# Kernel optimization log

Hardware: AMD Instinct MI355X
Metric: run time of the kernel (lower is better)

The kernel has to match this reference:

```python
import jax, jax.numpy as jnp
import numpy as np

EPS = 1e-5


def conv2d(x, w, b, pad):
    # x: [B,C,H,W], w: [O,I,kh,kw]
    out = jax.lax.conv_general_dilated(
        x, w, window_strides=(1, 1), padding=[(pad, pad), (pad, pad)],
        dimension_numbers=('NCHW', 'OIHW', 'NCHW'))
    return out + b[None, :, None, None]


def bilinear_gather(xf, py, px, H, W):
    # xf: [B,C,H*W]; py,px: [B,H,W] float sampling positions
    # zero padding outside the image (torchvision deform_conv2d semantics)
    y0 = jnp.floor(py)
    x0 = jnp.floor(px)
    wy = py - y0
    wx = px - x0
    y0i = y0.astype(jnp.int32)
    x0i = x0.astype(jnp.int32)
    B, C = xf.shape[0], xf.shape[1]
    acc = jnp.zeros((B, C, H, W), xf.dtype)
    for dy, wyv in ((0, 1.0 - wy), (1, wy)):
        for dx, wxv in ((0, 1.0 - wx), (1, wx)):
            yi = y0i + dy
            xi = x0i + dx
            valid = ((yi >= 0) & (yi < H) & (xi >= 0) & (xi < W)).astype(xf.dtype)
            idx = jnp.clip(yi, 0, H - 1) * W + jnp.clip(xi, 0, W - 1)  # [B,H,W]
            g = jnp.take_along_axis(xf, idx.reshape(B, 1, H * W), axis=2)
            g = g.reshape(B, C, H, W)
            acc = acc + g * (wyv * wxv * valid)[:, None]
    return acc


def deform_conv2d(x, offset, w, b, k):
    # x: [B,C,H,W]; offset: [B,2*k*k,H,W] ((dy,dx) pairs per kernel tap)
    B, C, H, W = x.shape
    pad = k // 2
    gy = jnp.arange(H, dtype=x.dtype)[None, :, None]
    gx = jnp.arange(W, dtype=x.dtype)[None, None, :]
    xf = x.reshape(B, C, H * W)
    out = jnp.zeros((B, w.shape[0], H, W), x.dtype)
    for i in range(k):
        for j in range(k):
            kk = i * k + j
            py = gy + (i - pad) + offset[:, 2 * kk]
            px = gx + (j - pad) + offset[:, 2 * kk + 1]
            samp = bilinear_gather(xf, py, px, H, W)  # [B,C,H,W]
            out = out + jnp.einsum('bchw,oc->bohw', samp, w[:, :, i, j])
    return out + b[None, :, None, None]


def setup_inputs() -> dict:
    key = jax.random.key(0)
    ks = jax.random.split(key, 16)
    B, C, H, W = 4, 64, 192, 192
    k = 3
    hid = max(1, C // 16)
    d = {}
    d['x'] = jax.random.normal(ks[0], (B, C, H, W), jnp.float32)
    # offset-prediction conv (3x3, pad 1) -> 2*k*k channels
    d['off_w'] = jax.random.normal(ks[1], (2 * k * k, C, 3, 3), jnp.float32) * 0.02
    d['off_b'] = jax.random.normal(ks[2], (2 * k * k,), jnp.float32) * 0.02
    # deformable conv weights (C->C, kxk)
    d['dw'] = jax.random.normal(ks[3], (C, C, k, k), jnp.float32) * 0.05
    d['db'] = jax.random.normal(ks[4], (C,), jnp.float32) * 0.05
    # BatchNorm (eval: running stats)
    d['bn_gamma'] = jnp.ones((C,), jnp.float32) + 0.1 * jax.random.normal(ks[5], (C,), jnp.float32)
    d['bn_beta'] = 0.1 * jax.random.normal(ks[6], (C,), jnp.float32)
    d['bn_mean'] = 0.1 * jax.random.normal(ks[7], (C,), jnp.float32)
    d['bn_var'] = jnp.ones((C,), jnp.float32)
    # channel attention: 1x1 squeeze / excite
    d['ca_w1'] = jax.random.normal(ks[8], (hid, C, 1, 1), jnp.float32) * 0.1
    d['ca_b1'] = jnp.zeros((hid,), jnp.float32)
    d['ca_w2'] = jax.random.normal(ks[9], (C, hid, 1, 1), jnp.float32) * 0.1
    d['ca_b2'] = jnp.zeros((C,), jnp.float32)
    # spatial attention: 7x7 conv -> 1 channel
    d['sa_w'] = jax.random.normal(ks[10], (1, C, 7, 7), jnp.float32) * 0.02
    d['sa_b'] = jnp.zeros((1,), jnp.float32)
    return d


def reference(x, off_w, off_b, dw, db, bn_gamma, bn_beta, bn_mean, bn_var,
              ca_w1, ca_b1, ca_w2, ca_b2, sa_w, sa_b):
    k = 3
    # extract: DeformableConv2d + BatchNorm2d
    offset = conv2d(x, off_w, off_b, pad=1)
    h = deform_conv2d(x, offset, dw, db, k)
    inv = jax.lax.rsqrt(bn_var + EPS)
    h = (h - bn_mean[None, :, None, None]) * (bn_gamma * inv)[None, :, None, None] \
        + bn_beta[None, :, None, None]
    # channel attention
    pooled = jnp.mean(h, axis=(2, 3), keepdims=True)  # [B,C,1,1]
    cw = conv2d(pooled, ca_w1, ca_b1, pad=0)
    cw = jax.nn.relu(cw)
    cw = conv2d(cw, ca_w2, ca_b2, pad=0)
    cw = jax.nn.sigmoid(cw)
    h = h * cw
    # spatial attention (7x7 conv, pad 3)
    sw = jax.nn.sigmoid(conv2d(h, sa_w, sa_b, pad=3))  # [B,1,H,W]
    h = h * sw
    return h
```

## Files before the change

### kernel.cpp

```cpp
#include <hip/hip_runtime.h>
#include <hip/hip_bf16.h>

#define H_  192
#define W_  192
#define HW  36864
#define B_  4

typedef __attribute__((ext_vector_type(8))) short short8;
typedef __attribute__((ext_vector_type(4))) float f32x4;
typedef __attribute__((ext_vector_type(4))) unsigned int u32x4;
typedef unsigned short ushort_t;
typedef unsigned int uint_t;

__device__ __forceinline__ ushort_t f2bf(float v) {
    uint_t u = __builtin_bit_cast(uint_t, v);
    u += 0x7FFFu + ((u >> 16) & 1u);
    return (ushort_t)(u >> 16);
}
__device__ __forceinline__ float bflo(uint_t u) {
    uint_t w = u << 16; return __builtin_bit_cast(float, w);
}
__device__ __forceinline__ float bfhi(uint_t u) {
    uint_t w = u & 0xFFFF0000u; return __builtin_bit_cast(float, w);
}
__device__ __forceinline__ short8 zero8() {
    u32x4 z = {0u, 0u, 0u, 0u};
    return __builtin_bit_cast(short8, z);
}

__device__ __forceinline__ void glds16(const ushort_t* src, void* lds_base) {
    __builtin_amdgcn_global_load_lds(
        (const __attribute__((address_space(1))) void*)src,
        (__attribute__((address_space(3))) void*)lds_base, 16, 0, 0);
}

__global__ void prep_kernel(const float* __restrict__ dw, const float* __restrict__ db,
                            const float* __restrict__ g, const float* __restrict__ be,
                            const float* __restrict__ mu, const float* __restrict__ var,
                            const float* __restrict__ ow,
                            ushort_t* __restrict__ w_bf, ushort_t* __restrict__ w_off,
                            float* __restrict__ scale, float* __restrict__ shift) {
    int idx = blockIdx.x * 256 + threadIdx.x;
    if (idx < 36864) {
        int tap = idx >> 12, o = (idx >> 6) & 63, c = idx & 63;
        w_bf[idx] = f2bf(dw[(o * 64 + c) * 9 + tap]);
    }
    int idx2 = idx - 36864;
    if (idx2 >= 0 && idx2 < 18432) {
        int tap = idx2 >> 11, o = (idx2 >> 6) & 31, c = idx2 & 63;
        w_off[idx2] = (o < 18) ? f2bf(ow[(o * 64 + c) * 9 + tap]) : (ushort_t)0;
    }
    if (idx < 64) {
        float s = g[idx] * rsqrtf(var[idx] + 1e-5f);
        scale[idx] = s;
        shift[idx] = (db[idx] - mu[idx]) * s + be[idx];
    }
}

__global__ __launch_bounds__(256) void transpose_kernel(const float* __restrict__ x,
                                                        ushort_t* __restrict__ x_t) {
    __shared__ uint_t tlds[256 * 33];
    int tid = threadIdx.x;
    int b = blockIdx.x / 144;
    int p0 = (blockIdx.x % 144) * 256;
    ushort_t* ts = (ushort_t*)tlds;
    for (int c = 0; c < 64; ++c) {
        float v = x[((size_t)(b * 64 + c)) * HW + p0 + tid];
        ts[tid * 66 + c] = f2bf(v);
    }
    __syncthreads();
#pragma unroll
    for (int j = 0; j < 8; ++j) {
        int chunk = j * 256 + tid;
        int pl = chunk >> 3, s = chunk & 7;
        int bd = pl * 33 + s * 4;
        u32x4 v = {tlds[bd], tlds[bd + 1], tlds[bd + 2], tlds[bd + 3]};
        ((u32x4*)x_t)[(size_t)(b * HW + p0) * 8 + chunk] = v;
    }
}

__device__ __forceinline__ u32x4 prd(const ushort_t* patch, int q, int slot) {
    return *(const u32x4*)((const char*)patch + q * 128 + ((slot ^ (q & 7)) << 4));
}

__device__ __forceinline__ bool corner_setup2(float ody, float odx,
                                              int ybase, int xbase, int ytop, int xleft,
                                              int* q, int* g, float* w) {
    float py = (float)ybase + ody;
    float px = (float)xbase + odx;
    float fy = floorf(py), fx = floorf(px);
    int y0 = (int)fy, x0 = (int)fx;
    float wy = py - fy, wx = px - fx;
    int y0c = min(max(y0, 0), H_ - 1), y1c = min(max(y0 + 1, 0), H_ - 1);
    int x0c = min(max(x0, 0), W_ - 1), x1c = min(max(x0 + 1, 0), W_ - 1);
    float vy0 = (y0 >= 0 && y0 < H_) ? 1.f : 0.f;
    float vy1 = (y0 + 1 >= 0 && y0 + 1 < H_) ? 1.f : 0.f;
    float vx0 = (x0 >= 0 && x0 < W_) ? 1.f : 0.f;
    float vx1 = (x0 + 1 >= 0 && x0 + 1 < W_) ? 1.f : 0.f;
    w[0] = (1.f - wy) * (1.f - wx) * vy0 * vx0;
    w[1] = (1.f - wy) * wx * vy0 * vx1;
    w[2] = wy * (1.f - wx) * vy1 * vx0;
    w[3] = wy * wx * vy1 * vx1;
    g[0] = (y0c * W_ + x0c) * 64; g[1] = (y0c * W_ + x1c) * 64;
    g[2] = (y1c * W_ + x0c) * 64; g[3] = (y1c * W_ + x1c) * 64;
    int iy0 = y0c - ytop, iy1 = y1c - ytop;
    int ix0 = x0c - xleft, ix1 = x1c - xleft;
    q[0] = iy0 * 40 + ix0; q[1] = iy0 * 40 + ix1;
    q[2] = iy1 * 40 + ix0; q[3] = iy1 * 40 + ix1;
    return ((unsigned)iy0 <= 11u) & ((unsigned)iy1 <= 11u) &
           ((unsigned)ix0 <= 39u) & ((unsigned)ix1 <= 39u);
}

__device__ __forceinline__ short8 interp_compute(const u32x4* buf, const float* w) {
    short8 r;
#pragma unroll
    for (int q = 0; q < 4; ++q) {
        float lo = w[0] * bflo(buf[0][q]) + w[1] * bflo(buf[1][q]) +
                   w[2] * bflo(buf[2][q]) + w[3] * bflo(buf[3][q]);
        float hi = w[0] * bfhi(buf[0][q]) + w[1] * bfhi(buf[1][q]) +
                   w[2] * bfhi(buf[2][q]) + w[3] * bfhi(buf[3][q]);
        __hip_bfloat162 h2 = __float22bfloat162_rn(make_float2(lo, hi));
        uint_t p;
        __builtin_memcpy(&p, &h2, 4);
        ((uint_t*)&r)[q] = p;
    }
    return r;
}

__global__ __launch_bounds__(384, 3) void deform_fused_kernel(
    const ushort_t* __restrict__ x_t, const ushort_t* __restrict__ w_off,
    const float* __restrict__ ob, const ushort_t* __restrict__ w_bf,
    const float* __restrict__ scale_g, const float* __restrict__ shift_g,
    float* __restrict__ out) {
    __shared__ __align__(16) ushort_t patch[480 * 64];

    int tid = threadIdx.x;
    int lane = tid & 63, w = tid >> 6;
    int tile = (blockIdx.x & 7) * 96 + (blockIdx.x >> 3);
    int b = tile / 192;
    int rem = tile % 192;
    int y0 = (rem / 6) * 6;
    int x0 = (rem % 6) * 32;
    int ytop = y0 - 3, xleft = x0 - 4;

    int ln = lane & 15, kg = lane >> 4;
    int yw = y0 + w;
    int xA = x0 + ln, xB = xA + 16;
    const ushort_t* xt_b = x_t + (size_t)b * (HW * 64);

    {
        char* pbase = (char*)patch;
#pragma unroll
        for (int t = 0; t < 10; ++t) {
            int g = t * 384 + tid;
            int q = g >> 3, sp = g & 7;
            int i = q / 40, j = q - i * 40;
            int pr = min(max(ytop + i, 0), H_ - 1);
            int pc = min(max(xleft + j, 0), W_ - 1);
            int s = sp ^ (q & 7);
            glds16(xt_b + (pr * W_ + pc) * 64 + s * 8, pbase + (t * 6 + w) * 1024);
        }
    }
    asm volatile("s_waitcnt vmcnt(0)" ::: "memory");
    __syncthreads();

    f32x4 ao[2][2];
#pragma unroll
    for (int i = 0; i < 2; ++i)
#pragma unroll
        for (int j = 0; j < 2; ++j) ao[i][j] = (f32x4){0.f, 0.f, 0.f, 0.f};

    for (int tap = 0; tap < 9; ++tap) {
        int ti = tap / 3 - 1, tj = tap % 3 - 1;
        bool vA = ((unsigned)(yw + ti) < (unsigned)H_) && ((unsigned)(xA + tj) < (unsigned)W_);
        bool vB = ((unsigned)(yw + ti) < (unsigned)H_) && ((unsigned)(xB + tj) < (unsigned)W_);
        int qA = (w + ti + 3) * 40 + (ln + 4 + tj);
        int qB = qA + 16;
        const ushort_t* wt = w_off + tap * 2048;
#pragma unroll
        for (int ks = 0; ks < 2; ++ks) {
            int ch = ks * 32 + kg * 8;
            int slot = kg + ks * 4;
            short8 a0 = *(const short8*)(wt + ln * 64 + ch);
            short8 a1 = *(const short8*)(wt + (16 + ln) * 64 + ch);
            short8 bA = vA ? __builtin_bit_cast(short8, prd(patch, qA, slot)) : zero8();
            short8 bB = vB ? __builtin_bit_cast(short8, prd(patch, qB, slot)) : zero8();
            ao[0][0] = __builtin_amdgcn_mfma_f32_16x16x32_bf16(a0, bA, ao[0][0], 0, 0, 0);
            ao[0][1] = __builtin_amdgcn_mfma_f32_16x16x32_bf16(a0, bB, ao[0][1], 0, 0, 0);
            ao[1][0] = __builtin_amdgcn_mfma_f32_16x16x32_bf16(a1, bA, ao[1][0], 0, 0, 0);
            ao[1][1] = __builtin_amdgcn_mfma_f32_16x16x32_bf16(a1, bB, ao[1][1], 0, 0, 0);
        }
    }

    float offA[18], offB[18];
#pragma unroll
    for (int m = 0; m < 18; ++m) {
        int src = (((m >> 2) & 3) << 4) | ln;
        float bias = ob[m];
        offA[m] = __shfl(ao[m >> 4][0][m & 3], src, 64) + bias;
        offB[m] = __shfl(ao[m >> 4][1][m & 3], src, 64) + bias;
    }

    f32x4 acc[4][2];
#pragma unroll
    for (int mt = 0; mt < 4; ++mt)
#pragma unroll
        for (int nt = 0; nt < 2; ++nt) acc[mt][nt] = (f32x4){0.f, 0.f, 0.f, 0.f};

#pragma unroll
    for (int tap = 0; tap < 9; ++tap) {
        int ti = tap / 3 - 1, tj = tap % 3 - 1;
        int qA[4], qB[4], gA[4], gB[4];
        float wA[4], wB[4];
        bool inA = corner_setup2(offA[2 * tap], offA[2 * tap + 1],
                                 yw + ti, xA + tj, ytop, xleft, qA, gA, wA);
        bool inB = corner_setup2(offB[2 * tap], offB[2 * tap + 1],
                                 yw + ti, xB + tj, ytop, xleft, qB, gB, wB);
        const ushort_t* wt = w_bf + tap * 4096;
#pragma unroll
        for (int ks = 0; ks < 2; ++ks) {
            int ch = ks * 32 + kg * 8;
            int slot = kg + ks * 4;
            u32x4 cA[4], cB[4];
            if (__builtin_expect(inA, 1)) {
#pragma unroll
                for (int c = 0; c < 4; ++c) cA[c] = prd(patch, qA[c], slot);
            } else {
#pragma unroll
                for (int c = 0; c < 4; ++c) cA[c] = *(const u32x4*)(xt_b + gA[c] + ch);
            }
            if (__builtin_expect(inB, 1)) {
#pragma unroll
                for (int c = 0; c < 4; ++c) cB[c] = prd(patch, qB[c], slot);
            } else {
#pragma unroll
                for (int c = 0; c < 4; ++c) cB[c] = *(const u32x4*)(xt_b + gB[c] + ch);
            }
            short8 fA = interp_compute(cA, wA);
            short8 fB = interp_compute(cB, wB);
            short8 a0 = *(const short8*)(wt + (0 + ln) * 64 + ch);
            short8 a1 = *(const short8*)(wt + (16 + ln) * 64 + ch);
            short8 a2 = *(const short8*)(wt + (32 + ln) * 64 + ch);
            short8 a3 = *(const short8*)(wt + (48 + ln) * 64 + ch);
            acc[0][0] = __builtin_amdgcn_mfma_f32_16x16x32_bf16(a0, fA, acc[0][0], 0, 0, 0);
            acc[0][1] = __builtin_amdgcn_mfma_f32_16x16x32_bf16(a0, fB, acc[0][1], 0, 0, 0);
            acc[1][0] = __builtin_amdgcn_mfma_f32_16x16x32_bf16(a1, fA, acc[1][0], 0, 0, 0);
            acc[1][1] = __builtin_amdgcn_mfma_f32_16x16x32_bf16(a1, fB, acc[1][1], 0, 0, 0);
            acc[2][0] = __builtin_amdgcn_mfma_f32_16x16x32_bf16(a2, fA, acc[2][0], 0, 0, 0);
            acc[2][1] = __builtin_amdgcn_mfma_f32_16x16x32_bf16(a2, fB, acc[2][1], 0, 0, 0);
            acc[3][0] = __builtin_amdgcn_mfma_f32_16x16x32_bf16(a3, fA, acc[3][0], 0, 0, 0);
            acc[3][1] = __builtin_amdgcn_mfma_f32_16x16x32_bf16(a3, fB, acc[3][1], 0, 0, 0);
        }
    }

#pragma unroll
    for (int mt = 0; mt < 4; ++mt) {
#pragma unroll
        for (int r = 0; r < 4; ++r) {
            int m = mt * 16 + kg * 4 + r;
            float sc = scale_g[m], sh = shift_g[m];
            size_t orow = (size_t)(b * 64 + m) * HW + yw * 192 + x0 + ln;
            out[orow] = acc[mt][0][r] * sc + sh;
            out[orow + 16] = acc[mt][1][r] * sc + sh;
        }
    }
}

__global__ __launch_bounds__(256) void pool_kernel(const float* __restrict__ h,
                                                   float* __restrict__ pooled) {
    __shared__ float red[4];
    int tid = threadIdx.x;
    const float* src = h + (size_t)blockIdx.x * HW;
    float s = 0.f;
#pragma unroll 4
    for (int i = tid * 4; i < HW; i += 1024) {
        float4 v = *(const float4*)(src + i);
        s += v.x + v.y + v.z + v.w;
    }
#pragma unroll
    for (int d = 1; d < 64; d <<= 1) s += __shfl_xor(s, d, 64);
    if ((tid & 63) == 0) red[tid >> 6] = s;
    __syncthreads();
    if (tid == 0)
        pooled[blockIdx.x] = (red[0] + red[1] + red[2] + red[3]) * (1.0f / (float)HW);
}

__global__ void ca_kernel(const float* __restrict__ pooled_g,
                          const float* __restrict__ w1, const float* __restrict__ b1,
                          const float* __restrict__ w2, const float* __restrict__ b2,
                          const float* __restrict__ saw, float* __restrict__ cw,
                          ushort_t* __restrict__ we_bf) {
    __shared__ float pooled[256];
    __shared__ float t1[16];
    int t = threadIdx.x;
    int b = t >> 6, o = t & 63;
    pooled[t] = pooled_g[t];
    __syncthreads();
    if (t < 16) {
        int bb = t >> 2, hh = t & 3;
        float a = b1[hh];
        for (int c = 0; c < 64; ++c) a += pooled[bb * 64 + c] * w1[hh * 64 + c];
        t1[t] = fmaxf(a, 0.f);
    }
    __syncthreads();
    float a = b2[o];
#pragma unroll
    for (int h2 = 0; h2 < 4; ++h2) a += t1[b * 4 + h2] * w2[o * 4 + h2];
    float cwv = 1.f / (1.f + __expf(-a));
    cw[t] = cwv;
    for (int tap = 0; tap < 64; ++tap) {
        float v = (tap < 49) ? cwv * saw[o * 49 + tap] : 0.f;
        we_bf[(b * 64 + tap) * 64 + o] = f2bf(v);
    }
}

__global__ __launch_bounds__(256) void tap_gemm_kernel(
    const float* __restrict__ h, const ushort_t* __restrict__ we_bf,
    ushort_t* __restrict__ u) {
    int tid = threadIdx.x;
    int b = blockIdx.y;
    int p0 = blockIdx.x * 128;
    int wid = tid >> 6, lane = tid & 63, ln = lane & 15, kg = lane >> 4;
    int pA = p0 + wid * 32 + ln, pB = pA + 16;
    const float* hb = h + (size_t)b * 64 * HW;
    const ushort_t* wt = we_bf + b * 4096;

    f32x4 acc[4][2];
#pragma unroll
    for (int mt = 0; mt < 4; ++mt)
#pragma unroll
        for (int nt = 0; nt < 2; ++nt) acc[mt][nt] = (f32x4){0.f, 0.f, 0.f, 0.f};

#pragma unroll
    for (int ks = 0; ks < 2; ++ks) {
        int ch = ks * 32 + kg * 8;
        short8 fA, fB;
#pragma unroll
        for (int q = 0; q < 8; ++q) {
            fA[q] = (short)f2bf(hb[(size_t)(ch + q) * HW + pA]);
            fB[q] = (short)f2bf(hb[(size_t)(ch + q) * HW + pB]);
        }
        short8 a0 = *(const short8*)(wt + (0 + ln) * 64 + ch);
        short8 a1 = *(const short8*)(wt + (16 + ln) * 64 + ch);
        short8 a2 = *(const short8*)(wt + (32 + ln) * 64 + ch);
        short8 a3 = *(const short8*)(wt + (48 + ln) * 64 + ch);
        acc[0][0] = __builtin_amdgcn_mfma_f32_16x16x32_bf16(a0, fA, acc[0][0], 0, 0, 0);
        acc[0][1] = __builtin_amdgcn_mfma_f32_16x16x32_bf16(a0, fB, acc[0][1], 0, 0, 0);
        acc[1][0] = __builtin_amdgcn_mfma_f32_16x16x32_bf16(a1, fA, acc[1][0], 0, 0, 0);
        acc[1][1] = __builtin_amdgcn_mfma_f32_16x16x32_bf16(a1, fB, acc[1][1], 0, 0, 0);
        acc[2][0] = __builtin_amdgcn_mfma_f32_16x16x32_bf16(a2, fA, acc[2][0], 0, 0, 0);
        acc[2][1] = __builtin_amdgcn_mfma_f32_16x16x32_bf16(a2, fB, acc[2][1], 0, 0, 0);
        acc[3][0] = __builtin_amdgcn_mfma_f32_16x16x32_bf16(a3, fA, acc[3][0], 0, 0, 0);
        acc[3][1] = __builtin_amdgcn_mfma_f32_16x16x32_bf16(a3, fB, acc[3][1], 0, 0, 0);
    }
#pragma unroll
    for (int mt = 0; mt < 4; ++mt)
#pragma unroll
        for (int r = 0; r < 4; ++r) {
            int m = mt * 16 + kg * 4 + r;
            if (m < 49) {
                ushort_t* up = u + (size_t)(b * 49 + m) * HW;
                up[pA] = f2bf(acc[mt][0][r]);
                up[pB] = f2bf(acc[mt][1][r]);
            }
        }
}

__global__ __launch_bounds__(256) void sa_final_kernel(
    float* __restrict__ out, const ushort_t* __restrict__ u,
    const float* __restrict__ cw, const float* __restrict__ sab) {
    __shared__ float cw_l[64];
    int tid = threadIdx.x;
    int b = blockIdx.y;
    int p = blockIdx.x * 256 + tid;
    if (tid < 64) cw_l[tid] = cw[b * 64 + tid];
    __syncthreads();
    int y = p / 192, x = p - y * 192;
    float s = sab[0];
    const ushort_t* ub = u + (size_t)b * 49 * HW;
#pragma unroll
    for (int dy = 0; dy < 7; ++dy)
#pragma unroll
        for (int dx = 0; dx < 7; ++dx) {
            int yy = y + dy - 3, xx = x + dx - 3;
            bool ok = ((unsigned)yy < 192u) && ((unsigned)xx < 192u);
            int ad = ok ? (p + (dy - 3) * 192 + (dx - 3)) : 0;
            float v = bflo((uint_t)ub[(size_t)(dy * 7 + dx) * HW + ad]);
            s += ok ? v : 0.f;
        }
    float swv = 1.f / (1.f + __expf(-s));
#pragma unroll 8
    for (int c = 0; c < 64; ++c) {
        size_t ix = (size_t)(b * 64 + c) * HW + p;
        out[ix] = out[ix] * (cw_l[c] * swv);
    }
}

extern "C" void kernel_launch(void* const* d_in, const int* in_sizes, int n_in,
                              void* d_out, int out_size, void* d_ws, size_t ws_size,
                              hipStream_t stream) {
    const float* x     = (const float*)d_in[0];
    const float* off_w = (const float*)d_in[1];
    const float* off_b = (const float*)d_in[2];
    const float* dw    = (const float*)d_in[3];
    const float* db    = (const float*)d_in[4];
    const float* bn_g  = (const float*)d_in[5];
    const float* bn_b  = (const float*)d_in[6];
    const float* bn_m  = (const float*)d_in[7];
    const float* bn_v  = (const float*)d_in[8];
    const float* ca_w1 = (const float*)d_in[9];
    const float* ca_b1 = (const float*)d_in[10];
    const float* ca_w2 = (const float*)d_in[11];
    const float* ca_b2 = (const float*)d_in[12];
    const float* sa_w  = (const float*)d_in[13];
    const float* sa_b  = (const float*)d_in[14];
    float* out = (float*)d_out;
    float* ws  = (float*)d_ws;

    ushort_t* x_t    = (ushort_t*)ws;
    ushort_t* u      = (ushort_t*)ws;
    ushort_t* w_bf   = (ushort_t*)(ws + 4718592);
    ushort_t* w_off  = (ushort_t*)(ws + 4737024);
    ushort_t* we_bf  = (ushort_t*)(ws + 4737024);
    float* scale     = ws + 4746240;
    float* shift     = ws + 4746304;
    float* cw        = ws + 4746368;
    float* pooled    = ws + 4746624;

    prep_kernel<<<216, 256, 0, stream>>>(dw, db, bn_g, bn_b, bn_m, bn_v, off_w,
                                         w_bf, w_off, scale, shift);
    transpose_kernel<<<576, 256, 0, stream>>>(x, x_t);
    deform_fused_kernel<<<768, 384, 0, stream>>>(x_t, w_off, off_b, w_bf,
                                                 scale, shift, out);
    pool_kernel<<<256, 256, 0, stream>>>(out, pooled);
    ca_kernel<<<1, 256, 0, stream>>>(pooled, ca_w1, ca_b1, ca_w2, ca_b2, sa_w, cw, we_bf);
    tap_gemm_kernel<<<dim3(288, 4), 256, 0, stream>>>(out, we_bf, u);
    sa_final_kernel<<<dim3(144, 4), 256, 0, stream>>>(out, u, cw, sa_b);
}
```

Measured before the change: 142.3 us.

## Enlarge deform conv tile to 6x48 pixels with 9 waves per block

The fused deformable-conv kernel now covers a 6x48 output tile with 576 threads (9 waves) instead of a 6x32 tile with 384 threads. The shared-memory halo patch grows to 12x56 pixels. Each wave's 32 pixels are remapped into row/column positions inside the tile. The aim is to shrink the halo overhead per output pixel and raise the share of bilinear samples that hit the patch. In exchange, LDS use per block rises, occupancy drops to 2 blocks per CU, and the grid shrinks to 512 blocks, which may load-balance worse across CUs.

Result: no change. 143.1 us (+0.5%).

```diff
diff --git a/kernel.cpp b/kernel.cpp
--- a/kernel.cpp
+++ b/kernel.cpp
@@ -105,10 +105,10 @@
     g[2] = (y1c * W_ + x0c) * 64; g[3] = (y1c * W_ + x1c) * 64;
     int iy0 = y0c - ytop, iy1 = y1c - ytop;
     int ix0 = x0c - xleft, ix1 = x1c - xleft;
-    q[0] = iy0 * 40 + ix0; q[1] = iy0 * 40 + ix1;
-    q[2] = iy1 * 40 + ix0; q[3] = iy1 * 40 + ix1;
+    q[0] = iy0 * 56 + ix0; q[1] = iy0 * 56 + ix1;
+    q[2] = iy1 * 56 + ix0; q[3] = iy1 * 56 + ix1;
     return ((unsigned)iy0 <= 11u) & ((unsigned)iy1 <= 11u) &
-           ((unsigned)ix0 <= 39u) & ((unsigned)ix1 <= 39u);
+           ((unsigned)ix0 <= 55u) & ((unsigned)ix1 <= 55u);
 }
 
 __device__ __forceinline__ short8 interp_compute(const u32x4* buf, const float* w) {
@@ -127,38 +127,44 @@
     return r;
 }
 
-__global__ __launch_bounds__(384, 3) void deform_fused_kernel(
+__global__ __launch_bounds__(576, 2) void deform_fused_kernel(
     const ushort_t* __restrict__ x_t, const ushort_t* __restrict__ w_off,
     const float* __restrict__ ob, const ushort_t* __restrict__ w_bf,
     const float* __restrict__ scale_g, const float* __restrict__ shift_g,
     float* __restrict__ out) {
-    __shared__ __align__(16) ushort_t patch[480 * 64];
+    __shared__ __align__(16) ushort_t patch[672 * 64];
 
     int tid = threadIdx.x;
     int lane = tid & 63, w = tid >> 6;
-    int tile = (blockIdx.x & 7) * 96 + (blockIdx.x >> 3);
-    int b = tile / 192;
-    int rem = tile % 192;
-    int y0 = (rem / 6) * 6;
-    int x0 = (rem % 6) * 32;
+    int tile = (blockIdx.x & 7) * 64 + (blockIdx.x >> 3);
+    int b = tile / 128;
+    int rem = tile % 128;
+    int y0 = (rem >> 2) * 6;
+    int x0 = (rem & 3) * 48;
     int ytop = y0 - 3, xleft = x0 - 4;
 
     int ln = lane & 15, kg = lane >> 4;
-    int yw = y0 + w;
-    int xA = x0 + ln, xB = xA + 16;
+    int locA = w * 32 + ln, locB = locA + 16;
+    int rowA = locA / 48, colA = locA - rowA * 48;
+    int rowB = locB / 48, colB = locB - rowB * 48;
+    int yA = y0 + rowA, xA = x0 + colA;
+    int yB = y0 + rowB, xB = x0 + colB;
     const ushort_t* xt_b = x_t + (size_t)b * (HW * 64);
 
     {
         char* pbase = (char*)patch;
 #pragma unroll
         for (int t = 0; t < 10; ++t) {
-            int g = t * 384 + tid;
-            int q = g >> 3, sp = g & 7;
-            int i = q / 40, j = q - i * 40;
-            int pr = min(max(ytop + i, 0), H_ - 1);
-            int pc = min(max(xleft + j, 0), W_ - 1);
-            int s = sp ^ (q & 7);
-            glds16(xt_b + (pr * W_ + pc) * 64 + s * 8, pbase + (t * 6 + w) * 1024);
+            if (t * 576 + w * 64 < 5376) {
+                int g = t * 576 + tid;
+                int q = g >> 3, sp = g & 7;
+                int i = q / 56, j = q - i * 56;
+                int pr = min(max(ytop + i, 0), H_ - 1);
+                int pc = min(max(xleft + j, 0), W_ - 1);
+                int s = sp ^ (q & 7);
+                glds16(xt_b + (pr * W_ + pc) * 64 + s * 8,
+                       pbase + (size_t)(t * 576 + w * 64) * 16);
+            }
         }
     }
     asm volatile("s_waitcnt vmcnt(0)" ::: "memory");
@@ -172,10 +178,10 @@
 
     for (int tap = 0; tap < 9; ++tap) {
         int ti = tap / 3 - 1, tj = tap % 3 - 1;
-        bool vA = ((unsigned)(yw + ti) < (unsigned)H_) && ((unsigned)(xA + tj) < (unsigned)W_);
-        bool vB = ((unsigned)(yw + ti) < (unsigned)H_) && ((unsigned)(xB + tj) < (unsigned)W_);
-        int qA = (w + ti + 3) * 40 + (ln + 4 + tj);
-        int qB = qA + 16;
+        bool vA = ((unsigned)(yA + ti) < (unsigned)H_) && ((unsigned)(xA + tj) < (unsigned)W_);
+        bool vB = ((unsigned)(yB + ti) < (unsigned)H_) && ((unsigned)(xB + tj) < (unsigned)W_);
+        int qA = (rowA + 3 + ti) * 56 + (colA + 4 + tj);
+        int qB = (rowB + 3 + ti) * 56 + (colB + 4 + tj);
         const ushort_t* wt = w_off + tap * 2048;
 #pragma unroll
         for (int ks = 0; ks < 2; ++ks) {
@@ -213,9 +219,9 @@
         int qA[4], qB[4], gA[4], gB[4];
         float wA[4], wB[4];
         bool inA = corner_setup2(offA[2 * tap], offA[2 * tap + 1],
-                                 yw + ti, xA + tj, ytop, xleft, qA, gA, wA);
+                                 yA + ti, xA + tj, ytop, xleft, qA, gA, wA);
         bool inB = corner_setup2(offB[2 * tap], offB[2 * tap + 1],
-                                 yw + ti, xB + tj, ytop, xleft, qB, gB, wB);
+                                 yB + ti, xB + tj, ytop, xleft, qB, gB, wB);
         const ushort_t* wt = w_bf + tap * 4096;
 #pragma unroll
         for (int ks = 0; ks < 2; ++ks) {
@@ -253,15 +259,17 @@
         }
     }
 
+    int pixA = yA * W_ + xA;
+    int pixB = yB * W_ + xB;
 #pragma unroll
     for (int mt = 0; mt < 4; ++mt) {
 #pragma unroll
         for (int r = 0; r < 4; ++r) {
             int m = mt * 16 + kg * 4 + r;
             float sc = scale_g[m], sh = shift_g[m];
-            size_t orow = (size_t)(b * 64 + m) * HW + yw * 192 + x0 + ln;
-            out[orow] = acc[mt][0][r] * sc + sh;
-            out[orow + 16] = acc[mt][1][r] * sc + sh;
+            size_t obase = (size_t)(b * 64 + m) * HW;
+            out[obase + pixA] = acc[mt][0][r] * sc + sh;
+            out[obase + pixB] = acc[mt][1][r] * sc + sh;
         }
     }
 }
@@ -430,7 +438,7 @@
     prep_kernel<<<216, 256, 0, stream>>>(dw, db, bn_g, bn_b, bn_m, bn_v, off_w,
                                          w_bf, w_off, scale, shift);
     transpose_kernel<<<576, 256, 0, stream>>>(x, x_t);
-    deform_fused_kernel<<<768, 384, 0, stream>>>(x_t, w_off, off_b, w_bf,
+    deform_fused_kernel<<<512, 576, 0, stream>>>(x_t, w_off, off_b, w_bf,
                                                  scale, shift, out);
     pool_kernel<<<256, 256, 0, stream>>>(out, pooled);
     ca_kernel<<<1, 256, 0, stream>>>(pooled, ca_w1, ca_b1, ca_w2, ca_b2, sa_w, cw, we_bf);
```
